# Kernel optimization log

Hardware: AMD Instinct MI355X
Metric: run time of the kernel (lower is better)

The kernel has to match this reference:

```python
import jax, jax.numpy as jnp
import numpy as np


def setup_inputs() -> dict:
    key = jax.random.key(0)
    k1, k2, k3, k4 = jax.random.split(key, 4)
    B, T, C, H = 4, 4096, 1024, 64
    x = jax.random.normal(k1, (B, T, C), dtype=jnp.float32)
    # nn.Linear weights, stored as (in, out) for x @ W
    s = 1.0 / np.sqrt(C)
    Wk = jax.random.uniform(k2, (C, H), dtype=jnp.float32, minval=-s, maxval=s)
    Wq = jax.random.uniform(k3, (C, H), dtype=jnp.float32, minval=-s, maxval=s)
    Wv = jax.random.uniform(k4, (C, H), dtype=jnp.float32, minval=-s, maxval=s)
    return {"x": x, "Wk": Wk, "Wq": Wq, "Wv": Wv}


def reference(x, Wk, Wq, Wv):
    # single-head causal self-attention (dropout=0 / eval mode)
    B, T, C = x.shape
    k = x @ Wk  # [B,T,H]
    q = x @ Wq  # [B,T,H]
    v = x @ Wv  # [B,T,H]
    scale = k.shape[-1] ** -0.5
    wei = jnp.einsum('bth,bsh->bts', q, k) * scale  # [B,T,T]
    causal = jnp.tril(jnp.ones((T, T), dtype=bool))
    wei = jnp.where(causal, wei, -jnp.inf)
    wei = jax.nn.softmax(wei, axis=-1)
    out = jnp.einsum('bts,bsh->bth', wei, v)  # [B,T,H]
    return out
```

## Files before the change

kernel.cpp:

```cpp
#include <hip/hip_runtime.h>
#include <hip/hip_bf16.h>

#define B_ 4
#define T_ 4096
#define C_ 1024
#define H_ 64
#define M_ (B_ * T_)
#define UPB 272

typedef __bf16 bf16x8 __attribute__((ext_vector_type(8)));
typedef float f32x8 __attribute__((ext_vector_type(8)));
typedef float f32x4 __attribute__((ext_vector_type(4)));
typedef unsigned short us8 __attribute__((ext_vector_type(8)));
typedef unsigned short us4 __attribute__((ext_vector_type(4)));

#define QSCALE 0.18033688011112042f
#define OFF2   23.083120654223414f

__device__ __forceinline__ unsigned short f2bf(float x) {
    return __builtin_bit_cast(unsigned short, (__bf16)x);
}
__device__ __forceinline__ float bf2f(unsigned short u) {
    return __builtin_bit_cast(float, (unsigned)u << 16);
}
__device__ __forceinline__ f32x4 mfma16(bf16x8 a, bf16x8 b, f32x4 c) {
    return __builtin_amdgcn_mfma_f32_16x16x32_bf16(a, b, c, 0, 0, 0);
}
__device__ __forceinline__ bf16x8 ldb8(const unsigned short* p) {
    return __builtin_bit_cast(bf16x8, *reinterpret_cast<const us8*>(p));
}
__device__ __forceinline__ bf16x8 ldlds8(const char* p) {
    return __builtin_bit_cast(bf16x8, *reinterpret_cast<const us8*>(p));
}
__device__ __forceinline__ void gll16(const void* g, char* ldsdst) {
    __builtin_amdgcn_global_load_lds(
        (const __attribute__((address_space(1))) unsigned*)g,
        (__attribute__((address_space(3))) unsigned*)ldsdst, 16, 0, 0);
}

__global__ __launch_bounds__(256) void wt_kernel(const float* __restrict__ Wk,
                                                 const float* __restrict__ Wq,
                                                 const float* __restrict__ Wv,
                                                 unsigned short* __restrict__ Wt) {
    __shared__ float t[64][65];
    const int wid = blockIdx.x >> 4;
    const int kb = (blockIdx.x & 15) * 64;
    const float* W = (wid == 0) ? Wk : (wid == 1 ? Wq : Wv);
    const int ty = threadIdx.x >> 6;
    const int tx = threadIdx.x & 63;
#pragma unroll
    for (int i = 0; i < 16; ++i) {
        int kl = i * 4 + ty;
        t[kl][tx] = W[(size_t)(kb + kl) * H_ + tx];
    }
    __syncthreads();
#pragma unroll
    for (int i = 0; i < 16; ++i) {
        int hl = i * 4 + ty;
        Wt[(size_t)(wid * 64 + hl) * C_ + kb + tx] = f2bf(t[tx][hl]);
    }
}

__global__ __launch_bounds__(256) void proj_kernel(const float* __restrict__ x,
                                                   const unsigned short* __restrict__ Wt,
                                                   unsigned short* __restrict__ Kb,
                                                   unsigned short* __restrict__ Qb,
                                                   unsigned short* __restrict__ Vt) {
    __shared__ char lds[61440];
    const int tid = threadIdx.x;
    const int w = tid >> 6, l = tid & 63;
    const int lg = l >> 4, cl = l & 15;
    const int mbase = blockIdx.x * 64;
    const int w64 = w << 6;

    f32x4 acc[12];
#pragma unroll
    for (int i = 0; i < 12; ++i) acc[i] = (f32x4){0.f, 0.f, 0.f, 0.f};

#define STAGE(AO, BO, KC)                                                        \
    {                                                                            \
        _Pragma("unroll") for (int i = 0; i < 2; ++i) {                          \
            int unit = i * 256 + tid;                                            \
            int row = unit >> 3, up = unit & 7;                                  \
            int lu = up ^ (row & 7);                                             \
            gll16(x + (size_t)(mbase + row) * C_ + (KC) + lu * 4,                \
                  lds + (AO) + (unsigned)(i * 256 + w64) * 16);                  \
        }                                                                        \
        _Pragma("unroll") for (int i = 0; i < 3; ++i) {                          \
            int unit = i * 256 + tid;                                            \
            int pr = unit >> 3, up = unit & 7;                                   \
            int u = up ^ (pr & 7);                                               \
            int r = pr * 2 + (u >> 2);                                           \
            gll16(Wt + (size_t)r * C_ + (KC) + (u & 3) * 8,                      \
                  lds + (BO) + (unsigned)(i * 256 + w64) * 16);                  \
        }                                                                        \
    }

#define COMPUTE(AO, BO)                                                          \
    {                                                                            \
        const int arow = w * 16 + cl;                                            \
        const int asw = cl & 7;                                                  \
        f32x4 alo = *reinterpret_cast<const f32x4*>(                             \
            lds + (AO) + arow * 128 + ((lg * 2) ^ asw) * 16);                    \
        f32x4 ahi = *reinterpret_cast<const f32x4*>(                             \
            lds + (AO) + arow * 128 + ((lg * 2 + 1) ^ asw) * 16);                \
        f32x8 af;                                                                \
        af[0] = alo[0]; af[1] = alo[1]; af[2] = alo[2]; af[3] = alo[3];          \
        af[4] = ahi[0]; af[5] = ahi[1]; af[6] = ahi[2]; af[7] = ahi[3];          \
        bf16x8 a = __builtin_convertvector(af, bf16x8);                          \
        _Pragma("unroll") for (int nf = 0; nf < 12; ++nf) {                      \
            int r = nf * 16 + cl;                                                \
            int pr = r >> 1;                                                     \
            bf16x8 bb = __builtin_bit_cast(bf16x8,                               \
                *reinterpret_cast<const us8*>(                                   \
                    lds + (BO) + pr * 128 +                                      \
                    ((((cl & 1) << 2) + lg) ^ (pr & 7)) * 16));                  \
            acc[nf] = mfma16(a, bb, acc[nf]);                                    \
        }                                                                        \
    }

    int a0 = 0, a1 = 8192, a2 = 16384;
    int b0 = 24576, b1 = 36864, b2 = 49152;

    STAGE(a0, b0, 0);
    STAGE(a1, b1, 32);
    for (int t = 0; t < 30; ++t) {
        asm volatile("s_waitcnt vmcnt(5)" ::: "memory");
        asm volatile("s_barrier" ::: "memory");
        STAGE(a2, b2, (t + 2) * 32);
        COMPUTE(a0, b0);
        int ta = a0; a0 = a1; a1 = a2; a2 = ta;
        int tb = b0; b0 = b1; b1 = b2; b2 = tb;
    }
    asm volatile("s_waitcnt vmcnt(5)" ::: "memory");
    asm volatile("s_barrier" ::: "memory");
    COMPUTE(a0, b0);
    asm volatile("s_waitcnt vmcnt(0)" ::: "memory");
    asm volatile("s_barrier" ::: "memory");
    COMPUTE(a1, b1);
#undef STAGE
#undef COMPUTE

    const int rbase = mbase + w * 16 + lg * 4;
#pragma unroll
    for (int nf = 0; nf < 12; ++nf) {
        int colg = nf * 16 + cl;
#pragma unroll
        for (int r = 0; r < 4; ++r) {
            float v = acc[nf][r];
            int m = rbase + r;
            if (colg < 64) {
                Kb[m * H_ + colg] = f2bf(v);
            } else if (colg < 128) {
                Qb[m * H_ + (colg - 64)] = f2bf(v * QSCALE);
            } else {
                int b = m >> 12, t = m & 4095, h = colg - 128;
                Vt[((b << 6) + h) * T_ + t] = f2bf(v);
            }
        }
    }
}

__global__ __launch_bounds__(256, 2) void attn_kernel(const unsigned short* __restrict__ Qb,
                                                      const unsigned short* __restrict__ Kb,
                                                      const unsigned short* __restrict__ Vt,
                                                      float* __restrict__ out,
                                                      unsigned short* __restrict__ Opart,
                                                      float* __restrict__ lpart) {
    __shared__ char lds[49152];
    const int tid = threadIdx.x;
    const int w = tid >> 6, l = tid & 63;
    const int lg = l >> 4, cl = l & 15;
    const int kgrp = lg * 8;
    char* pb = lds + 32768 + w * 4096;

    const int lin = blockIdx.x;
    const int xcd = lin & 7;
    const int b = xcd >> 1;
    const int f = (xcd & 1) * 136 + (lin >> 3);

    int qt = 0, Sp = 0;
    while (f >= Sp + ((qt + 2) >> 1)) { Sp += (qt + 2) >> 1; ++qt; }
    const int chunk = f - Sp;
    const int nc = (qt + 2) >> 1;

    const int qbase = qt * 128;
    const int qw = qbase + w * 32;
    const int s0 = chunk * 256;
    int s1 = s0 + 256;
    if (s1 > qbase + 128) s1 = qbase + 128;
    const int ntile = (s1 - s0) >> 6;

    const unsigned short* q0 = Qb + (size_t)(b * T_ + qw + cl) * H_;
    bf16x8 qa00 = ldb8(q0 + kgrp), qa01 = ldb8(q0 + 32 + kgrp);
    bf16x8 qa10 = ldb8(q0 + 16 * H_ + kgrp), qa11 = ldb8(q0 + 16 * H_ + 32 + kgrp);

    f32x4 o[2][4];
#pragma unroll
    for (int rf = 0; rf < 2; ++rf)
#pragma unroll
        for (int nf = 0; nf < 4; ++nf) o[rf][nf] = (f32x4){0.f, 0.f, 0.f, 0.f};
    float lrow0 = 0.f, lrow1 = 0.f;

#define STG(KO, VO, SB)                                                          \
    {                                                                            \
        _Pragma("unroll") for (int i = 0; i < 2; ++i) {                          \
            int u = i * 256 + tid;                                               \
            int row = u >> 3, up = u & 7;                                        \
            int lu = up ^ (row & 7);                                             \
            gll16(Kb + (size_t)(b * T_ + (SB) + row) * H_ + lu * 8,              \
                  lds + (KO) + (unsigned)(i * 256 + (w << 6)) * 16);             \
            gll16(Vt + (size_t)((b << 6) + row) * T_ + (SB) + lu * 8,            \
                  lds + (VO) + (unsigned)(i * 256 + (w << 6)) * 16);             \
        }                                                                        \
    }

    int k0o = 0, k1o = 8192;
    int v0o = 16384, v1o = 24576;

    STG(k0o, v0o, s0);
    for (int t = 0; t < ntile; ++t) {
        const int sbase = s0 + t * 64;
        asm volatile("s_waitcnt vmcnt(0)" ::: "memory");
        asm volatile("s_barrier" ::: "memory");
        if (t + 1 < ntile) STG(k1o, v1o, sbase + 64);

        if (qw + 31 >= sbase) {
            f32x4 sA[4], sB[4];
            __builtin_amdgcn_s_setprio(1);
#pragma unroll
            for (int nf = 0; nf < 4; ++nf) {
                const int row = nf * 16 + cl, sw = row & 7;
                bf16x8 k0v = ldlds8(lds + k0o + row * 128 + (lg ^ sw) * 16);
                bf16x8 k1v = ldlds8(lds + k0o + row * 128 + ((4 + lg) ^ sw) * 16);
                f32x4 z = (f32x4){0.f, 0.f, 0.f, 0.f};
                sA[nf] = mfma16(k1v, qa01, mfma16(k0v, qa00, z));
                sB[nf] = mfma16(k1v, qa11, mfma16(k0v, qa10, z));
            }
            __builtin_amdgcn_s_setprio(0);
            if (sbase + 63 > qw) {
#pragma unroll
                for (int nf = 0; nf < 4; ++nf) {
#pragma unroll
                    for (int r = 0; r < 4; ++r) {
                        const int kv = sbase + nf * 16 + lg * 4 + r;
                        const int qA = qw + cl;
                        if (kv > qA)      sA[nf][r] = -1e30f;
                        if (kv > qA + 16) sB[nf][r] = -1e30f;
                    }
                }
            }
            {
                const int sw = (cl & 7) << 4;
#pragma unroll
                for (int nf = 0; nf < 4; ++nf) {
                    us4 vA, vB;
#pragma unroll
                    for (int r = 0; r < 4; ++r) {
                        float pA = exp2f(sA[nf][r] - OFF2);
                        float pB = exp2f(sB[nf][r] - OFF2);
                        lrow0 += pA;
                        lrow1 += pB;
                        vA[r] = f2bf(pA);
                        vB[r] = f2bf(pB);
                    }
                    const int colb = nf * 32 + lg * 8;
                    *reinterpret_cast<us4*>(pb + ((cl * 128 + colb) ^ sw)) = vA;
                    *reinterpret_cast<us4*>(pb + (((16 + cl) * 128 + colb) ^ sw)) = vB;
                }
            }
            const int msk = (cl & 7) << 4;
            bf16x8 pa00 = ldlds8(pb + ((cl * 128 + lg * 16) ^ msk));
            bf16x8 pa01 = ldlds8(pb + ((cl * 128 + 64 + lg * 16) ^ msk));
            bf16x8 pa10 = ldlds8(pb + (((16 + cl) * 128 + lg * 16) ^ msk));
            bf16x8 pa11 = ldlds8(pb + (((16 + cl) * 128 + 64 + lg * 16) ^ msk));
            __builtin_amdgcn_s_setprio(1);
#pragma unroll
            for (int nf = 0; nf < 4; ++nf) {
                const int row = nf * 16 + cl, sw = row & 7;
                bf16x8 v0 = ldlds8(lds + v0o + row * 128 + (lg ^ sw) * 16);
                bf16x8 v1 = ldlds8(lds + v0o + row * 128 + ((4 + lg) ^ sw) * 16);
                o[0][nf] = mfma16(pa01, v1, mfma16(pa00, v0, o[0][nf]));
                o[1][nf] = mfma16(pa11, v1, mfma16(pa10, v0, o[1][nf]));
            }
            __builtin_amdgcn_s_setprio(0);
        }
        int tk = k0o; k0o = k1o; k1o = tk;
        int tv = v0o; v0o = v1o; v1o = tv;
    }
#undef STG

    lrow0 += __shfl_xor(lrow0, 16);
    lrow0 += __shfl_xor(lrow0, 32);
    lrow1 += __shfl_xor(lrow1, 16);
    lrow1 += __shfl_xor(lrow1, 32);

    if (nc == 1) {
#pragma unroll
        for (int rf = 0; rf < 2; ++rf) {
            float lr = rf ? lrow1 : lrow0;
            float inv[4];
#pragma unroll
            for (int r = 0; r < 4; ++r) inv[r] = 1.0f / __shfl(lr, lg * 4 + r);
#pragma unroll
            for (int nf = 0; nf < 4; ++nf)
#pragma unroll
                for (int r = 0; r < 4; ++r) {
                    int t = qw + rf * 16 + lg * 4 + r;
                    out[(size_t)(b * T_ + t) * H_ + nf * 16 + cl] =
                        o[rf][nf][r] * inv[r];
                }
        }
    } else {
        const int slot = b * UPB + f;
        unsigned short* Ob = Opart + (size_t)slot * 8192;
#pragma unroll
        for (int rf = 0; rf < 2; ++rf)
#pragma unroll
            for (int nf = 0; nf < 4; ++nf) {
                us4 v;
#pragma unroll
                for (int r = 0; r < 4; ++r) v[r] = f2bf(o[rf][nf][r]);
                *reinterpret_cast<us4*>(Ob + ((w * 8 + rf * 4 + nf) * 64 + l) * 4) = v;
            }
        if (lg == 0) {
            lpart[slot * 128 + w * 32 + cl] = lrow0;
            lpart[slot * 128 + w * 32 + 16 + cl] = lrow1;
        }
    }
}

__global__ __launch_bounds__(256) void combine_kernel(const unsigned short* __restrict__ Opart,
                                                      const float* __restrict__ lpart,
                                                      float* __restrict__ out) {
    const int qt = 2 + blockIdx.x;
    const int b = blockIdx.y;
    const int c = (qt + 2) >> 1;
    const int slot0 = b * UPB + ((qt + 1) * (qt + 1)) / 4;

    const int p = blockIdx.z * 4 + (threadIdx.x >> 6);
    const int l = threadIdx.x & 63;
    const int wq = p >> 3, rf = (p >> 2) & 1, nf = p & 3;
    const int lg = l >> 4, cl = l & 15;

    float a[4] = {0.f, 0.f, 0.f, 0.f};
    float ls[4] = {0.f, 0.f, 0.f, 0.f};
    for (int j = 0; j < c; ++j) {
        const unsigned short* src =
            Opart + (size_t)(slot0 + j) * 8192 + (p * 64 + l) * 4;
        us4 v = *reinterpret_cast<const us4*>(src);
        const float* lp = lpart + (slot0 + j) * 128 + wq * 32 + rf * 16 + lg * 4;
#pragma unroll
        for (int e = 0; e < 4; ++e) {
            a[e] += bf2f(v[e]);
            ls[e] += lp[e];
        }
    }
#pragma unroll
    for (int e = 0; e < 4; ++e) {
        int row = qt * 128 + wq * 32 + rf * 16 + lg * 4 + e;
        out[(size_t)(b * T_ + row) * H_ + nf * 16 + cl] = a[e] / ls[e];
    }
}

extern "C" void kernel_launch(void* const* d_in, const int* in_sizes, int n_in,
                              void* d_out, int out_size, void* d_ws, size_t ws_size,
                              hipStream_t stream) {
    const float* x  = (const float*)d_in[0];
    const float* Wk = (const float*)d_in[1];
    const float* Wq = (const float*)d_in[2];
    const float* Wv = (const float*)d_in[3];
    float* out = (float*)d_out;

    char* ws = (char*)d_ws;
    unsigned short* Kb = (unsigned short*)(ws);
    unsigned short* Qb = (unsigned short*)(ws + 2097152);
    unsigned short* Vt = (unsigned short*)(ws + 2 * 2097152);
    unsigned short* Wt = (unsigned short*)(ws + 3 * 2097152);
    const size_t base = 6684672ull;
    unsigned short* Opart = (unsigned short*)(ws + base);
    float* lpart = (float*)(ws + base + (size_t)B_ * UPB * 16384);

    wt_kernel<<<dim3(48), dim3(256), 0, stream>>>(Wk, Wq, Wv, Wt);
    proj_kernel<<<dim3(256), dim3(256), 0, stream>>>(x, Wt, Kb, Qb, Vt);
    attn_kernel<<<dim3(8 * 136), dim3(256), 0, stream>>>(
        Qb, Kb, Vt, out, Opart, lpart);
    combine_kernel<<<dim3(30, B_, 8), dim3(256), 0, stream>>>(Opart, lpart, out);
}
```

Before: 57.10 us.

## Split projection output columns across two blocks and specialize load waves

The projection kernel now launches twice as many blocks. Each block computes half of the 192 output columns (K+Q or the second half covering Q+V), which shrinks per-block LDS and accumulator registers. Block indices are remapped so that the two column halves of an x tile land together for L2 locality. Staging is warp-specialized: two waves load the x tile and two load the weight tile, each with its own vmcnt wait. The cost is that the x tile is read twice from memory, in exchange for better CU occupancy on a 256-CU device.

```diff
diff --git a/kernel.cpp b/kernel.cpp
--- a/kernel.cpp
+++ b/kernel.cpp
@@ -66,85 +66,98 @@
                                                    unsigned short* __restrict__ Kb,
                                                    unsigned short* __restrict__ Qb,
                                                    unsigned short* __restrict__ Vt) {
-    __shared__ char lds[61440];
+    __shared__ char lds[43008];
     const int tid = threadIdx.x;
     const int w = tid >> 6, l = tid & 63;
     const int lg = l >> 4, cl = l & 15;
-    const int mbase = blockIdx.x * 64;
-    const int w64 = w << 6;
-
-    f32x4 acc[12];
-#pragma unroll
-    for (int i = 0; i < 12; ++i) acc[i] = (f32x4){0.f, 0.f, 0.f, 0.f};
-
-#define STAGE(AO, BO, KC)                                                        \
+
+    const int lin = blockIdx.x;
+    const int work = (lin & 7) * 64 + (lin >> 3);
+    const int g = work & 1;
+    const int mbase = (work >> 1) * 64;
+
+    f32x4 acc[6];
+#pragma unroll
+    for (int i = 0; i < 6; ++i) acc[i] = (f32x4){0.f, 0.f, 0.f, 0.f};
+
+#define STAGE(BUF, KC)                                                           \
     {                                                                            \
-        _Pragma("unroll") for (int i = 0; i < 2; ++i) {                          \
-            int unit = i * 256 + tid;                                            \
-            int row = unit >> 3, up = unit & 7;                                  \
-            int lu = up ^ (row & 7);                                             \
-            gll16(x + (size_t)(mbase + row) * C_ + (KC) + lu * 4,                \
-                  lds + (AO) + (unsigned)(i * 256 + w64) * 16);                  \
+        if (w < 2) {                                                             \
+            _Pragma("unroll") for (int i = 0; i < 4; ++i) {                      \
+                int ub = i * 128 + w * 64;                                       \
+                int u = ub + l;                                                  \
+                int row = u >> 3, up = u & 7;                                    \
+                int lu = up ^ (row & 7);                                         \
+                gll16(x + (size_t)(mbase + row) * C_ + (KC) + lu * 4,            \
+                      lds + (BUF) + (unsigned)ub * 16);                          \
+            }                                                                    \
+        } else {                                                                 \
+            _Pragma("unroll") for (int i = 0; i < 3; ++i) {                      \
+                int ub = i * 128 + (w - 2) * 64;                                 \
+                int u = ub + l;                                                  \
+                int pr = u >> 3, up = u & 7;                                     \
+                int uu = up ^ (pr & 7);                                          \
+                int r = g * 96 + pr * 2 + (uu >> 2);                             \
+                gll16(Wt + (size_t)r * C_ + (KC) + (uu & 3) * 8,                 \
+                      lds + (BUF) + 8192 + (unsigned)ub * 16);                   \
+            }                                                                    \
         }                                                                        \
-        _Pragma("unroll") for (int i = 0; i < 3; ++i) {                          \
-            int unit = i * 256 + tid;                                            \
-            int pr = unit >> 3, up = unit & 7;                                   \
-            int u = up ^ (pr & 7);                                               \
-            int r = pr * 2 + (u >> 2);                                           \
-            gll16(Wt + (size_t)r * C_ + (KC) + (u & 3) * 8,                      \
-                  lds + (BO) + (unsigned)(i * 256 + w64) * 16);                  \
-        }                                                                        \
-    }
-
-#define COMPUTE(AO, BO)                                                          \
+    }
+
+#define VWAIT()                                                                  \
+    {                                                                            \
+        if (w < 2) { asm volatile("s_waitcnt vmcnt(4)" ::: "memory"); }          \
+        else       { asm volatile("s_waitcnt vmcnt(3)" ::: "memory"); }          \
+    }
+
+#define COMPUTE(BUF)                                                             \
     {                                                                            \
         const int arow = w * 16 + cl;                                            \
         const int asw = cl & 7;                                                  \
         f32x4 alo = *reinterpret_cast<const f32x4*>(                             \
-            lds + (AO) + arow * 128 + ((lg * 2) ^ asw) * 16);                    \
+            lds + (BUF) + arow * 128 + ((lg * 2) ^ asw) * 16);                   \
         f32x4 ahi = *reinterpret_cast<const f32x4*>(                             \
-            lds + (AO) + arow * 128 + ((lg * 2 + 1) ^ asw) * 16);                \
+            lds + (BUF) + arow * 128 + ((lg * 2 + 1) ^ asw) * 16);               \
         f32x8 af;                                                                \
         af[0] = alo[0]; af[1] = alo[1]; af[2] = alo[2]; af[3] = alo[3];          \
         af[4] = ahi[0]; af[5] = ahi[1]; af[6] = ahi[2]; af[7] = ahi[3];          \
         bf16x8 a = __builtin_convertvector(af, bf16x8);                          \
-        _Pragma("unroll") for (int nf = 0; nf < 12; ++nf) {                      \
-            int r = nf * 16 + cl;                                                \
-            int pr = r >> 1;                                                     \
+        _Pragma("unroll") for (int nf = 0; nf < 6; ++nf) {                       \
+            int rl = nf * 16 + cl;                                               \
+            int pr = rl >> 1;                                                    \
             bf16x8 bb = __builtin_bit_cast(bf16x8,                               \
                 *reinterpret_cast<const us8*>(                                   \
-                    lds + (BO) + pr * 128 +                                      \
+                    lds + (BUF) + 8192 + pr * 128 +                              \
                     ((((cl & 1) << 2) + lg) ^ (pr & 7)) * 16));                  \
             acc[nf] = mfma16(a, bb, acc[nf]);                                    \
         }                                                                        \
     }
 
-    int a0 = 0, a1 = 8192, a2 = 16384;
-    int b0 = 24576, b1 = 36864, b2 = 49152;
-
-    STAGE(a0, b0, 0);
-    STAGE(a1, b1, 32);
+    int u0 = 0, u1 = 14336, u2 = 28672;
+
+    STAGE(u0, 0);
+    STAGE(u1, 32);
     for (int t = 0; t < 30; ++t) {
-        asm volatile("s_waitcnt vmcnt(5)" ::: "memory");
+        VWAIT();
         asm volatile("s_barrier" ::: "memory");
-        STAGE(a2, b2, (t + 2) * 32);
-        COMPUTE(a0, b0);
-        int ta = a0; a0 = a1; a1 = a2; a2 = ta;
-        int tb = b0; b0 = b1; b1 = b2; b2 = tb;
-    }
-    asm volatile("s_waitcnt vmcnt(5)" ::: "memory");
+        STAGE(u2, (t + 2) * 32);
+        COMPUTE(u0);
+        int tu = u0; u0 = u1; u1 = u2; u2 = tu;
+    }
+    VWAIT();
     asm volatile("s_barrier" ::: "memory");
-    COMPUTE(a0, b0);
+    COMPUTE(u0);
     asm volatile("s_waitcnt vmcnt(0)" ::: "memory");
     asm volatile("s_barrier" ::: "memory");
-    COMPUTE(a1, b1);
+    COMPUTE(u1);
 #undef STAGE
+#undef VWAIT
 #undef COMPUTE
 
     const int rbase = mbase + w * 16 + lg * 4;
 #pragma unroll
-    for (int nf = 0; nf < 12; ++nf) {
-        int colg = nf * 16 + cl;
+    for (int nf = 0; nf < 6; ++nf) {
+        int colg = g * 96 + nf * 16 + cl;
 #pragma unroll
         for (int r = 0; r < 4; ++r) {
             float v = acc[nf][r];
@@ -382,7 +395,7 @@
     float* lpart = (float*)(ws + base + (size_t)B_ * UPB * 16384);
 
     wt_kernel<<<dim3(48), dim3(256), 0, stream>>>(Wk, Wq, Wv, Wt);
-    proj_kernel<<<dim3(256), dim3(256), 0, stream>>>(x, Wt, Kb, Qb, Vt);
+    proj_kernel<<<dim3(512), dim3(256), 0, stream>>>(x, Wt, Kb, Qb, Vt);
     attn_kernel<<<dim3(8 * 136), dim3(256), 0, stream>>>(
         Qb, Kb, Vt, out, Opart, lpart);
     combine_kernel<<<dim3(30, B_, 8), dim3(256), 0, stream>>>(Opart, lpart, out);
```

Result: no change. 56.88 us (-0.4%).
